# Kernel optimization log

Hardware: AMD Instinct MI355X
Metric: run time of the kernel (lower is better)

The kernel has to match this reference:

```python
import jax, jax.numpy as jnp
import numpy as np

N_NODES = 50000
N_EDGES = 1600000
IN_F, H_F, N_C = 128, 128, 16
NEG_SLOPE = 0.2  # DGL GATConv default


def setup_inputs() -> dict:
    key = jax.random.key(0)
    ks = jax.random.split(key, 12)
    def w(k, shape, fan_in):
        return jax.random.normal(k, shape, jnp.float32) / np.float32(np.sqrt(fan_in))
    return {
        "feat": jax.random.normal(ks[0], (N_NODES, IN_F), jnp.float32),
        "src": jax.random.randint(ks[1], (N_EDGES,), 0, N_NODES, dtype=jnp.int32),
        "dst": jax.random.randint(ks[2], (N_EDGES,), 0, N_NODES, dtype=jnp.int32),
        "W1": w(ks[3], (IN_F, H_F), IN_F), "al1": w(ks[4], (H_F,), H_F), "ar1": w(ks[5], (H_F,), H_F), "b1": jnp.zeros((H_F,), jnp.float32),
        "W2": w(ks[6], (H_F, H_F), H_F), "al2": w(ks[7], (H_F,), H_F), "ar2": w(ks[8], (H_F,), H_F), "b2": jnp.zeros((H_F,), jnp.float32),
        "W3": w(ks[9], (H_F, N_C), H_F), "al3": w(ks[10], (N_C,), N_C), "ar3": w(ks[11], (N_C,), N_C), "b3": jnp.zeros((N_C,), jnp.float32),
    }


def _gat_layer(h, src, dst, W, al, ar, b):
    # DGL GATConv (1 head): ft = W h; e_ij = LeakyReLU(a_l.ft_src + a_r.ft_dst);
    # alpha = edge_softmax over incoming edges of dst; out = sum alpha * ft_src + bias
    ft = h @ W                                   # [N, out]
    el = ft @ al                                 # [N]
    er = ft @ ar                                 # [N]
    e = jax.nn.leaky_relu(el[src] + er[dst], negative_slope=NEG_SLOPE)  # [E]
    emax = jax.ops.segment_max(e, dst, num_segments=N_NODES)
    emax = jnp.where(jnp.isfinite(emax), emax, 0.0)  # guard isolated nodes
    ex = jnp.exp(e - emax[dst])                  # [E]
    esum = jax.ops.segment_sum(ex, dst, num_segments=N_NODES)  # [N]
    agg = jax.ops.segment_sum(ex[:, None] * ft[src], dst, num_segments=N_NODES)  # [N, out]
    out = agg / jnp.where(esum > 0, esum, 1.0)[:, None] + b
    return jax.nn.relu(out)


def reference(feat, src, dst, W1, al1, ar1, b1, W2, al2, ar2, b2, W3, al3, ar3, b3):
    h = _gat_layer(feat, src, dst, W1, al1, ar1, b1)
    h = _gat_layer(h, src, dst, W2, al2, ar2, b2)
    h = _gat_layer(h, src, dst, W3, al3, ar3, b3)
    return h  # [N_NODES, N_C]
```

## Files before the change

kernel.cpp:

```cpp
#include <hip/hip_runtime.h>
#include <hip/hip_bf16.h>

#define NN 50000
#define NE 1600000
#define FF 128
#define CC 16
#define NB ((NN + 63) / 64)
#define NBLK 256
#define CH ((NE + NBLK - 1) / NBLK)

using bf16 = __hip_bfloat16;
using bf16x8 = __attribute__((ext_vector_type(8))) short;
using f32x4  = __attribute__((ext_vector_type(4))) float;

static __device__ __forceinline__ float ldf(const void* p, int i, int isbf){
    return isbf ? __bfloat162float(((const bf16*)p)[i]) : ((const float*)p)[i];
}
static __device__ __forceinline__ float bflo(unsigned u){
    union{unsigned x; float f;} c; c.x = u << 16; return c.f;
}
static __device__ __forceinline__ float bfhi(unsigned u){
    union{unsigned x; float f;} c; c.x = u & 0xFFFF0000u; return c.f;
}
static __device__ __forceinline__ float rdlanef(float v, int l){
    return __int_as_float(__builtin_amdgcn_readlane(__float_as_int(v), l));
}
static __device__ __forceinline__ unsigned short f2bfu(float v){
    bf16 b = __float2bfloat16(v);
    union{bf16 b; unsigned short u;} c; c.b = b; return c.u;
}

__global__ __launch_bounds__(256) void k_prep(const unsigned short* __restrict__ featu,
                                              const void* __restrict__ W1, const void* __restrict__ W2,
                                              const void* __restrict__ W3, int* __restrict__ dflag,
                                              int* __restrict__ bcounts, unsigned short* __restrict__ wtg){
    __shared__ int cnt;
    const int t = threadIdx.x;
    if (t == 0) cnt = 0;
    __syncthreads();
    unsigned short lo = featu[2 * t];
    int e = (lo >> 7) & 0xFF;
    if (e >= 117 && e <= 137) atomicAdd(&cnt, 1);
    __syncthreads();
    const int isbf = (cnt >= 128) ? 1 : 0;
    int idx = blockIdx.x * 256 + t;
    if (idx == 0) *dflag = isbf;
    if (idx < NB) bcounts[idx] = 0;
    if (idx < 32768){
        int l = idx >> 14;
        int e2 = idx & 16383;
        int f = e2 >> 7, k = e2 & 127;
        const void* W = l ? W2 : W1;
        wtg[idx] = f2bfu(ldf(W, k * FF + f, isbf));
    } else if (idx < 34816){
        int e2 = idx - 32768;
        int f = e2 >> 7, k = e2 & 127;
        wtg[idx] = f2bfu(ldf(W3, k * CC + f, isbf));
    }
}


__global__ __launch_bounds__(256) void k_bcount(const int* __restrict__ dst, int* __restrict__ bcounts,
                                                int* __restrict__ bh){
    __shared__ int hist[NB];
    const int t = threadIdx.x, b = blockIdx.x;
    for (int i = t; i < NB; i += 256) hist[i] = 0;
    __syncthreads();
    const int beg = b * CH, end = (beg + CH < NE) ? beg + CH : NE;
    for (int i = beg + t; i < end; i += 256){
        int d = dst[i];
        if ((unsigned)d >= NN) d = 0;
        atomicAdd(&hist[d >> 6], 1);
    }
    __syncthreads();
    for (int k = t; k < NB; k += 256){
        int v = hist[k];
        bh[k * NBLK + b] = v;
        if (v) atomicAdd(&bcounts[k], v);
    }
}

__global__ __launch_bounds__(256) void k_bscan(const int* __restrict__ bcounts, int* __restrict__ bbase,
                                               int* __restrict__ rowptr){
    __shared__ int s[256];
    const int t = threadIdx.x;
    constexpr int PT = (NB + 255) / 256;
    int loc[PT];
    int sum = 0;
    #pragma unroll
    for (int i = 0; i < PT; i++){
        int idx = t * PT + i;
        int v = (idx < NB) ? bcounts[idx] : 0;
        loc[i] = sum;
        sum += v;
    }
    s[t] = sum; __syncthreads();
    for (int off = 1; off < 256; off <<= 1){
        int x = (t >= off) ? s[t - off] : 0;
        __syncthreads();
        s[t] += x;
        __syncthreads();
    }
    int base = (t > 0) ? s[t - 1] : 0;
    #pragma unroll
    for (int i = 0; i < PT; i++){
        int idx = t * PT + i;
        if (idx < NB) bbase[idx] = base + loc[i];
    }
    if (t == 255){
        bbase[NB] = s[255];
        rowptr[NN] = s[255];
    }
}

__global__ __launch_bounds__(256) void k_boffset(const int* __restrict__ bbase, int* __restrict__ bh){
    int k = blockIdx.x * 4 + (threadIdx.x >> 6);
    int lane = threadIdx.x & 63;
    if (k >= NB) return;
    int v[4];
    int s = 0;
    #pragma unroll
    for (int i = 0; i < 4; i++){
        v[i] = bh[k * NBLK + 4 * lane + i];
        s += v[i];
    }
    int tot = s;
    #pragma unroll
    for (int off = 1; off < 64; off <<= 1){
        int x = __shfl_up(s, off);
        if (lane >= off) s += x;
    }
    int run = bbase[k] + s - tot;
    #pragma unroll
    for (int i = 0; i < 4; i++){
        bh[k * NBLK + 4 * lane + i] = run;
        run += v[i];
    }
}

__global__ __launch_bounds__(256) void k_bucket(const int* __restrict__ src, const int* __restrict__ dst,
                                                const int* __restrict__ bh, unsigned* __restrict__ bpairs){
    __shared__ int cur[NB];
    const int t = threadIdx.x, b = blockIdx.x;
    for (int k = t; k < NB; k += 256) cur[k] = bh[k * NBLK + b];
    __syncthreads();
    const int beg = b * CH, end = (beg + CH < NE) ? beg + CH : NE;
    for (int i = beg + t; i < end; i += 256){
        int s = src[i];
        int d = dst[i];
        if ((unsigned)s >= NN) s = 0;
        if ((unsigned)d >= NN) d = 0;
        int p = atomicAdd(&cur[d >> 6], 1);
        if ((unsigned)p < NE) bpairs[p] = (unsigned)s | ((unsigned)(d & 63) << 16);
    }
}

__global__ __launch_bounds__(256) void k_bsort(const unsigned* __restrict__ bpairs, const int* __restrict__ bbase,
                                               int* __restrict__ rowptr, int* __restrict__ csrsrc){
    __shared__ int cnt[64];
    __shared__ int cur[64];
    const int t = threadIdx.x;
    const int b = blockIdx.x;
    const int base = bbase[b];
    const int endb = bbase[b + 1];
    if (t < 64) cnt[t] = 0;
    __syncthreads();
    for (int i = base + t; i < endb; i += 256)
        atomicAdd(&cnt[bpairs[i] >> 16], 1);
    __syncthreads();
    if (t < 64){
        int v = cnt[t];
        int inc = v;
        #pragma unroll
        for (int off = 1; off < 64; off <<= 1){
            int x = __shfl_up(inc, off);
            if (t >= off) inc += x;
        }
        int excl = inc - v;
        cur[t] = excl;
        int d = b * 64 + t;
        if (d < NN) rowptr[d] = base + excl;
    }
    __syncthreads();
    for (int i = base + t; i < endb; i += 256){
        unsigned pr = bpairs[i];
        int p = atomicAdd(&cur[pr >> 16], 1);
        csrsrc[base + p] = (int)(pr & 0xFFFFu);
    }
}


template<bool XDYN>
__global__ __launch_bounds__(256) void k_mgemm(const void* __restrict__ X, const unsigned short* __restrict__ wtg,
                                               const void* __restrict__ al, const void* __restrict__ ar,
                                               const int* __restrict__ dflag, bf16* __restrict__ ft,
                                               float* __restrict__ el, float* __restrict__ er){
    const int isbf = *dflag;
    const int t  = threadIdx.x;
    const int n0 = blockIdx.x * 64;
    const int wv = t >> 6;
    const int lane = t & 63;
    const int quad = lane >> 4;
    const int mcol = lane & 15;
    const int row = n0 + wv * 16 + mcol;
    const int rc  = (row < NN) ? row : 0;

    bf16x8 afr[4];
    if (XDYN && !isbf){
        const float* xr = (const float*)X + rc * FF + quad * 8;
        #pragma unroll
        for (int kt = 0; kt < 4; kt++){
            float4 a = *(const float4*)(xr + kt * 32);
            float4 b = *(const float4*)(xr + kt * 32 + 4);
            union { bf16x8 v; unsigned u[4]; } c;
            c.u[0] = (unsigned)f2bfu(a.x) | ((unsigned)f2bfu(a.y) << 16);
            c.u[1] = (unsigned)f2bfu(a.z) | ((unsigned)f2bfu(a.w) << 16);
            c.u[2] = (unsigned)f2bfu(b.x) | ((unsigned)f2bfu(b.y) << 16);
            c.u[3] = (unsigned)f2bfu(b.z) | ((unsigned)f2bfu(b.w) << 16);
            afr[kt] = c.v;
        }
    } else {
        const unsigned short* xr = (const unsigned short*)X + rc * FF + quad * 8;
        #pragma unroll
        for (int kt = 0; kt < 4; kt++)
            afr[kt] = *(const bf16x8*)(xr + kt * 32);
    }

    float elp[4] = {0.f,0.f,0.f,0.f}, erp[4] = {0.f,0.f,0.f,0.f};

    #pragma unroll
    for (int f = 0; f < 8; f++){
        f32x4 acc = {0.f, 0.f, 0.f, 0.f};
        const unsigned short* wr = wtg + (f * 16 + mcol) * FF + quad * 8;
        #pragma unroll
        for (int kt = 0; kt < 4; kt++){
            bf16x8 bfr = *(const bf16x8*)(wr + kt * 32);
            acc = __builtin_amdgcn_mfma_f32_16x16x32_bf16(afr[kt], bfr, acc, 0, 0, 0);
        }
        int col = f * 16 + mcol;
        float alv = ldf(al, col, isbf);
        float arv = ldf(ar, col, isbf);
        #pragma unroll
        for (int reg = 0; reg < 4; reg++){
            int node = n0 + wv * 16 + quad * 4 + reg;
            float v = acc[reg];
            if (node < NN) ft[node * FF + col] = __float2bfloat16(v);
            elp[reg] += v * alv;
            erp[reg] += v * arv;
        }
    }

    #pragma unroll
    for (int reg = 0; reg < 4; reg++){
        float pl = elp[reg], pr = erp[reg];
        #pragma unroll
        for (int off = 1; off < 16; off <<= 1){
            pl += __shfl_xor(pl, off);
            pr += __shfl_xor(pr, off);
        }
        int node = n0 + wv * 16 + quad * 4 + reg;
        if (mcol == 0 && node < NN){ el[node] = pl; er[node] = pr; }
    }
}


__global__ __launch_bounds__(256) void k_mgemm3(const void* __restrict__ X, const unsigned short* __restrict__ wt3g,
                                                const void* __restrict__ al, const void* __restrict__ ar,
                                                const int* __restrict__ dflag, float* __restrict__ ft,
                                                float* __restrict__ el, float* __restrict__ er){
    const int isbf = *dflag;
    const int t  = threadIdx.x;
    const int n0 = blockIdx.x * 64;
    const int wv = t >> 6;
    const int lane = t & 63;
    const int quad = lane >> 4;
    const int mcol = lane & 15;
    const int row = n0 + wv * 16 + mcol;
    const int rc  = (row < NN) ? row : 0;

    const unsigned short* xr = (const unsigned short*)X + rc * FF + quad * 8;
    const unsigned short* wr = wt3g + mcol * FF + quad * 8;

    f32x4 acc = {0.f, 0.f, 0.f, 0.f};
    #pragma unroll
    for (int kt = 0; kt < 4; kt++){
        bf16x8 afr = *(const bf16x8*)(xr + kt * 32);
        bf16x8 bfr = *(const bf16x8*)(wr + kt * 32);
        acc = __builtin_amdgcn_mfma_f32_16x16x32_bf16(afr, bfr, acc, 0, 0, 0);
    }

    float alv = ldf(al, mcol, isbf);
    float arv = ldf(ar, mcol, isbf);
    #pragma unroll
    for (int reg = 0; reg < 4; reg++){
        int node = n0 + wv * 16 + quad * 4 + reg;
        float v = acc[reg];
        if (node < NN) ft[node * CC + mcol] = v;
        float pl = v * alv, pr = v * arv;
        #pragma unroll
        for (int off = 1; off < 16; off <<= 1){
            pl += __shfl_xor(pl, off);
            pr += __shfl_xor(pr, off);
        }
        if (mcol == 0 && node < NN){ el[node] = pl; er[node] = pr; }
    }
}


__global__ __launch_bounds__(256) void k_agg128(const void* __restrict__ ftv, const float* __restrict__ el,
                                                const float* __restrict__ er, const int* __restrict__ rowptr,
                                                const int* __restrict__ csrsrc, const void* __restrict__ bias,
                                                const int* __restrict__ dflag, unsigned* __restrict__ outp){
    const int isbf = *dflag;
    int lane = threadIdx.x & 63;
    int n = blockIdx.x * 4 + (threadIdx.x >> 6);
    if (n >= NN) return;
    int beg = rowptr[n], end = rowptr[n + 1];
    beg = (beg < 0) ? 0 : (beg > NE ? NE : beg);
    end = (end < beg) ? beg : (end > NE ? NE : end);
    int deg = end - beg;
    float erd = er[n];

    float m = -3.4e38f;
    int   s_c = 0;
    float e_c = 0.f;
    for (int i = beg + lane; i < end; i += 64){
        int s = csrsrc[i];
        if ((unsigned)s >= NN) s = 0;
        float e = el[s] + erd;
        e = (e >= 0.f) ? e : 0.2f * e;
        if (i < beg + 64){ s_c = s; e_c = e; }
        m = fmaxf(m, e);
    }
    #pragma unroll
    for (int off = 32; off; off >>= 1) m = fmaxf(m, __shfl_xor(m, off));

    int jmax = (deg < 64) ? deg : 64;
    float w_c = (lane < jmax) ? __expf(e_c - m) : 0.f;
    float lsum = w_c;
    #pragma unroll
    for (int off = 32; off; off >>= 1) lsum += __shfl_xor(lsum, off);

    const unsigned* ftb = (const unsigned*)ftv;
    float acc0 = 0.f, acc1 = 0.f;
    int j = 0;
    if (jmax >= 8){
        float w[8]; unsigned u[8];
        #pragma unroll
        for (int q = 0; q < 8; q++){
            int s = __builtin_amdgcn_readlane(s_c, q);
            w[q] = rdlanef(w_c, q);
            u[q] = (ftb + s * 64)[lane];
        }
        for (j = 8; j + 8 <= jmax; j += 8){
            float wn[8]; unsigned un[8];
            #pragma unroll
            for (int q = 0; q < 8; q++){
                int s = __builtin_amdgcn_readlane(s_c, j + q);
                wn[q] = rdlanef(w_c, j + q);
                un[q] = (ftb + s * 64)[lane];
            }
            #pragma unroll
            for (int q = 0; q < 8; q++){
                acc0 += w[q] * bflo(u[q]);
                acc1 += w[q] * bfhi(u[q]);
                w[q] = wn[q]; u[q] = un[q];
            }
        }
        #pragma unroll
        for (int q = 0; q < 8; q++){
            acc0 += w[q] * bflo(u[q]);
            acc1 += w[q] * bfhi(u[q]);
        }
    }
    for (; j < jmax; ++j){
        int s = __builtin_amdgcn_readlane(s_c, j);
        float w = rdlanef(w_c, j);
        unsigned u = (ftb + s * 64)[lane];
        acc0 += w * bflo(u); acc1 += w * bfhi(u);
    }
    for (int i = beg + 64; i < end; ++i){
        int s = csrsrc[i];
        if ((unsigned)s >= NN) s = 0;
        float e = el[s] + erd;
        e = (e >= 0.f) ? e : 0.2f * e;
        float w = __expf(e - m);
        unsigned u = (ftb + s * 64)[lane];
        lsum += w;
        acc0 += w * bflo(u); acc1 += w * bfhi(u);
    }
    float inv = 1.f / ((lsum > 0.f) ? lsum : 1.f);
    float o0 = fmaxf(acc0 * inv + ldf(bias, 2 * lane,     isbf), 0.f);
    float o1 = fmaxf(acc1 * inv + ldf(bias, 2 * lane + 1, isbf), 0.f);
    unsigned pk = (unsigned)f2bfu(o0) | ((unsigned)f2bfu(o1) << 16);
    outp[n * 64 + lane] = pk;
}


__global__ __launch_bounds__(256) void k_agg16(const float* __restrict__ ftv, const float* __restrict__ el,
                                               const float* __restrict__ er, const int* __restrict__ rowptr,
                                               const int* __restrict__ csrsrc, const void* __restrict__ bias,
                                               const int* __restrict__ dflag, void* __restrict__ outp){
    const int isbf = *dflag;
    int lane = threadIdx.x & 63;
    int n = blockIdx.x * 4 + (threadIdx.x >> 6);
    if (n >= NN) return;
    int beg = rowptr[n], end = rowptr[n + 1];
    beg = (beg < 0) ? 0 : (beg > NE ? NE : beg);
    end = (end < beg) ? beg : (end > NE ? NE : end);
    int deg = end - beg;
    float erd = er[n];

    float m = -3.4e38f;
    int   s_c = 0;
    float e_c = 0.f;
    for (int i = beg + lane; i < end; i += 64){
        int s = csrsrc[i];
        if ((unsigned)s >= NN) s = 0;
        float e = el[s] + erd;
        e = (e >= 0.f) ? e : 0.2f * e;
        if (i < beg + 64){ s_c = s; e_c = e; }
        m = fmaxf(m, e);
    }
    #pragma unroll
    for (int off = 32; off; off >>= 1) m = fmaxf(m, __shfl_xor(m, off));

    int jmax = (deg < 64) ? deg : 64;
    float w_c = (lane < jmax) ? __expf(e_c - m) : 0.f;
    float lsum = w_c;
    #pragma unroll
    for (int off = 32; off; off >>= 1) lsum += __shfl_xor(lsum, off);

    const float4* ftq = (const float4*)ftv;
    const int g   = lane >> 2;
    const int fl2 = lane & 3;
    int nbatch = (jmax + 15) >> 4;
    float wq[4]; float4 uq[4];
    #pragma unroll
    for (int q = 0; q < 4; q++){
        int eidx = (q * 16 + g) & 63;
        int s = __shfl(s_c, eidx);
        wq[q] = (q < nbatch) ? __shfl(w_c, eidx) : 0.f;
        uq[q] = ftq[(unsigned)s * 4 + fl2];
    }
    float a4[4] = {0.f,0.f,0.f,0.f};
    #pragma unroll
    for (int q = 0; q < 4; q++){
        a4[0] += wq[q] * uq[q].x;
        a4[1] += wq[q] * uq[q].y;
        a4[2] += wq[q] * uq[q].z;
        a4[3] += wq[q] * uq[q].w;
    }
    for (int i = beg + 64; i < end; ++i){
        int s = csrsrc[i];
        if ((unsigned)s >= NN) s = 0;
        float e = el[s] + erd;
        e = (e >= 0.f) ? e : 0.2f * e;
        float w = __expf(e - m);
        lsum += w;
        if (g == 0){
            float4 u = ftq[(unsigned)s * 4 + fl2];
            a4[0] += w * u.x; a4[1] += w * u.y; a4[2] += w * u.z; a4[3] += w * u.w;
        }
    }
    #pragma unroll
    for (int i = 0; i < 4; i++){
        a4[i] += __shfl_xor(a4[i], 4);
        a4[i] += __shfl_xor(a4[i], 8);
        a4[i] += __shfl_xor(a4[i], 16);
        a4[i] += __shfl_xor(a4[i], 32);
    }
    float inv = 1.f / ((lsum > 0.f) ? lsum : 1.f);
    if (lane < 4){
        float o0 = fmaxf(a4[0] * inv + ldf(bias, fl2 * 4 + 0, isbf), 0.f);
        float o1 = fmaxf(a4[1] * inv + ldf(bias, fl2 * 4 + 1, isbf), 0.f);
        float o2 = fmaxf(a4[2] * inv + ldf(bias, fl2 * 4 + 2, isbf), 0.f);
        float o3 = fmaxf(a4[3] * inv + ldf(bias, fl2 * 4 + 3, isbf), 0.f);
        if (isbf){
            uint2 pk;
            pk.x = (unsigned)f2bfu(o0) | ((unsigned)f2bfu(o1) << 16);
            pk.y = (unsigned)f2bfu(o2) | ((unsigned)f2bfu(o3) << 16);
            ((uint2*)outp)[n * 4 + fl2] = pk;
        } else {
            float4 o; o.x = o0; o.y = o1; o.z = o2; o.w = o3;
            ((float4*)outp)[n * 4 + fl2] = o;
        }
    }
}


static size_t align256(size_t x){ return (x + 255) & ~(size_t)255; }

extern "C" void kernel_launch(void* const* d_in, const int* in_sizes, int n_in,
                              void* d_out, int out_size, void* d_ws, size_t ws_size,
                              hipStream_t stream) {
    const void* feat = d_in[0];
    const int*  src  = (const int*)d_in[1];
    const int*  dst  = (const int*)d_in[2];
    const void* W1 = d_in[3];
    const void* al1= d_in[4];
    const void* ar1= d_in[5];
    const void* b1 = d_in[6];
    const void* W2 = d_in[7];
    const void* al2= d_in[8];
    const void* ar2= d_in[9];
    const void* b2 = d_in[10];
    const void* W3 = d_in[11];
    const void* al3= d_in[12];
    const void* ar3= d_in[13];
    const void* b3 = d_in[14];

    char* p = (char*)d_ws;
    size_t off = 0;
    auto carve = [&](size_t bytes)->void*{
        void* r = p + off;
        off += align256(bytes);
        return r;
    };
    float* ftA   = (float*)carve((size_t)NN * FF * 4);
    unsigned* hB = (unsigned*)carve((size_t)NN * FF * 4);
    float* el    = (float*)carve((size_t)NN * 4);
    float* er    = (float*)carve((size_t)NN * 4);
    int*   rowptr= (int*)  carve((size_t)(NN + 1) * 4);
    int*   csrsrc= (int*)  carve((size_t)NE * 4);
    int*   bcounts=(int*)  carve((size_t)NB * 4);
    int*   bbase  =(int*)  carve((size_t)(NB + 1) * 4);
    int*   bh     =(int*)  carve((size_t)NB * NBLK * 4);
    unsigned short* wtg = (unsigned short*)carve((size_t)34816 * 2);
    int*   dflag  =(int*)  carve(256);
    unsigned* bpairs = (unsigned*)hB;
    void*  ftb   = ftA;
    (void)ws_size; (void)n_in; (void)in_sizes; (void)out_size;

    dim3 b256(256);

    k_prep<<<dim3(136), b256, 0, stream>>>((const unsigned short*)feat, W1, W2, W3, dflag, bcounts, wtg);

    k_bcount<<<dim3(NBLK), b256, 0, stream>>>(dst, bcounts, bh);
    k_bscan<<<dim3(1), b256, 0, stream>>>(bcounts, bbase, rowptr);
    k_boffset<<<dim3((NB + 3) / 4), b256, 0, stream>>>(bbase, bh);
    k_bucket<<<dim3(NBLK), b256, 0, stream>>>(src, dst, bh, bpairs);
    k_bsort<<<dim3(NB), b256, 0, stream>>>(bpairs, bbase, rowptr, csrsrc);

    const int mg_grid   = (NN + 63) / 64;
    const int node_grid = (NN + 3) / 4;

    k_mgemm<true><<<dim3(mg_grid), b256, 0, stream>>>(feat, wtg, al1, ar1, dflag, (bf16*)ftb, el, er);
    k_agg128<<<dim3(node_grid), b256, 0, stream>>>(ftb, el, er, rowptr, csrsrc, b1, dflag, hB);

    k_mgemm<false><<<dim3(mg_grid), b256, 0, stream>>>(hB, wtg + 16384, al2, ar2, dflag, (bf16*)ftb, el, er);
    k_agg128<<<dim3(node_grid), b256, 0, stream>>>(ftb, el, er, rowptr, csrsrc, b2, dflag, hB);

    k_mgemm3<<<dim3(mg_grid), b256, 0, stream>>>(hB, wtg + 32768, al3, ar3, dflag, (float*)ftb, el, er);
    k_agg16<<<dim3(node_grid), b256, 0, stream>>>((const float*)ftb, el, er, rowptr, csrsrc, b3, dflag, d_out);
}
```

Before: 335.1 us.

## Gather four edges per wave with 16-byte loads in 128-wide aggregation

The 128-feature aggregation kernel now splits each wave into four 16-lane groups. Each group gathers a different neighbor's row with uint4 (8 bf16) loads, and the groups combine their partial sums with cross-lane shuffles at the end. This replaces per-lane 4-byte gathers handled one edge at a time, aiming at fewer, wider memory transactions and more edges in flight. The costs are extra shuffles, padding of the edge count to a multiple of four, and a tail loop for degree above 64 that uses only one quarter of the lanes.

After: 337.8 us. No clear change (+0.8%).

```diff
diff --git a/kernel.cpp b/kernel.cpp
--- a/kernel.cpp
+++ b/kernel.cpp
@@ -341,59 +341,73 @@
     #pragma unroll
     for (int off = 32; off; off >>= 1) lsum += __shfl_xor(lsum, off);
 
-    const unsigned* ftb = (const unsigned*)ftv;
-    float acc0 = 0.f, acc1 = 0.f;
-    int j = 0;
-    if (jmax >= 8){
-        float w[8]; unsigned u[8];
-        #pragma unroll
-        for (int q = 0; q < 8; q++){
-            int s = __builtin_amdgcn_readlane(s_c, q);
-            w[q] = rdlanef(w_c, q);
-            u[q] = (ftb + s * 64)[lane];
-        }
-        for (j = 8; j + 8 <= jmax; j += 8){
-            float wn[8]; unsigned un[8];
-            #pragma unroll
-            for (int q = 0; q < 8; q++){
-                int s = __builtin_amdgcn_readlane(s_c, j + q);
-                wn[q] = rdlanef(w_c, j + q);
-                un[q] = (ftb + s * 64)[lane];
+    const int g = lane >> 4;
+    const int c = lane & 15;
+    const uint4* ftq4 = (const uint4*)ftv;
+    float acc[8] = {0.f,0.f,0.f,0.f,0.f,0.f,0.f,0.f};
+    int jmax4 = (jmax + 3) & ~3;
+
+    for (int base = 0; base < jmax4; base += 16){
+        uint4 u[4];
+        float wB[4];
+        #pragma unroll
+        for (int q = 0; q < 4; q++){
+            int jj = base + q * 4;
+            if (jj < jmax4){
+                int idx = jj + g;
+                int sE = __shfl(s_c, idx);
+                wB[q] = __shfl(w_c, idx);
+                u[q] = ftq4[(unsigned)sE * 16u + c];
+            } else {
+                wB[q] = 0.f;
+                u[q] = (uint4){0u, 0u, 0u, 0u};
             }
-            #pragma unroll
-            for (int q = 0; q < 8; q++){
-                acc0 += w[q] * bflo(u[q]);
-                acc1 += w[q] * bfhi(u[q]);
-                w[q] = wn[q]; u[q] = un[q];
-            }
-        }
-        #pragma unroll
-        for (int q = 0; q < 8; q++){
-            acc0 += w[q] * bflo(u[q]);
-            acc1 += w[q] * bfhi(u[q]);
-        }
-    }
-    for (; j < jmax; ++j){
-        int s = __builtin_amdgcn_readlane(s_c, j);
-        float w = rdlanef(w_c, j);
-        unsigned u = (ftb + s * 64)[lane];
-        acc0 += w * bflo(u); acc1 += w * bfhi(u);
-    }
+        }
+        #pragma unroll
+        for (int q = 0; q < 4; q++){
+            float w = wB[q];
+            acc[0] += w * bflo(u[q].x); acc[1] += w * bfhi(u[q].x);
+            acc[2] += w * bflo(u[q].y); acc[3] += w * bfhi(u[q].y);
+            acc[4] += w * bflo(u[q].z); acc[5] += w * bfhi(u[q].z);
+            acc[6] += w * bflo(u[q].w); acc[7] += w * bfhi(u[q].w);
+        }
+    }
+
     for (int i = beg + 64; i < end; ++i){
         int s = csrsrc[i];
         if ((unsigned)s >= NN) s = 0;
         float e = el[s] + erd;
         e = (e >= 0.f) ? e : 0.2f * e;
         float w = __expf(e - m);
-        unsigned u = (ftb + s * 64)[lane];
         lsum += w;
-        acc0 += w * bflo(u); acc1 += w * bfhi(u);
-    }
-    float inv = 1.f / ((lsum > 0.f) ? lsum : 1.f);
-    float o0 = fmaxf(acc0 * inv + ldf(bias, 2 * lane,     isbf), 0.f);
-    float o1 = fmaxf(acc1 * inv + ldf(bias, 2 * lane + 1, isbf), 0.f);
-    unsigned pk = (unsigned)f2bfu(o0) | ((unsigned)f2bfu(o1) << 16);
-    outp[n * 64 + lane] = pk;
+        if (g == 0){
+            uint4 u = ftq4[(unsigned)s * 16u + c];
+            acc[0] += w * bflo(u.x); acc[1] += w * bfhi(u.x);
+            acc[2] += w * bflo(u.y); acc[3] += w * bfhi(u.y);
+            acc[4] += w * bflo(u.z); acc[5] += w * bfhi(u.z);
+            acc[6] += w * bflo(u.w); acc[7] += w * bfhi(u.w);
+        }
+    }
+
+    #pragma unroll
+    for (int k = 0; k < 8; k++){
+        acc[k] += __shfl_xor(acc[k], 16);
+        acc[k] += __shfl_xor(acc[k], 32);
+    }
+
+    if (g == 0){
+        float inv = 1.f / ((lsum > 0.f) ? lsum : 1.f);
+        float o[8];
+        #pragma unroll
+        for (int k = 0; k < 8; k++)
+            o[k] = fmaxf(acc[k] * inv + ldf(bias, c * 8 + k, isbf), 0.f);
+        uint4 pk;
+        pk.x = (unsigned)f2bfu(o[0]) | ((unsigned)f2bfu(o[1]) << 16);
+        pk.y = (unsigned)f2bfu(o[2]) | ((unsigned)f2bfu(o[3]) << 16);
+        pk.z = (unsigned)f2bfu(o[4]) | ((unsigned)f2bfu(o[5]) << 16);
+        pk.w = (unsigned)f2bfu(o[6]) | ((unsigned)f2bfu(o[7]) << 16);
+        ((uint4*)outp)[n * 16 + c] = pk;
+    }
 }
 
 
```

## Simplify CSR build to global atomic count-scan-scatter and drop max-subtraction in agg16

Applied to the files above, without the earlier changes.

Replaces the two-level bucketed CSR construction (block histograms, bucket offsets, bucket scatter, per-bucket sort) with a direct per-node global atomic count, a single-block scan, and an atomic scatter into csrsrc. The goal is fewer launches and fewer passes over the edge list. The trade is more contention on global atomics and a non-deterministic edge order. The final 16-wide aggregation kernel is also rewritten into a single pass that skips the softmax max subtraction, which risks exp overflow for large logits.

After: 513.8 us. 53.3% more time.

```diff
diff --git a/kernel.cpp b/kernel.cpp
--- a/kernel.cpp
+++ b/kernel.cpp
@@ -5,9 +5,7 @@
 #define NE 1600000
 #define FF 128
 #define CC 16
-#define NB ((NN + 63) / 64)
-#define NBLK 256
-#define CH ((NE + NBLK - 1) / NBLK)
+#define NCPAD 50176
 
 using bf16 = __hip_bfloat16;
 using bf16x8 = __attribute__((ext_vector_type(8))) short;
@@ -33,7 +31,7 @@
 __global__ __launch_bounds__(256) void k_prep(const unsigned short* __restrict__ featu,
                                               const void* __restrict__ W1, const void* __restrict__ W2,
                                               const void* __restrict__ W3, int* __restrict__ dflag,
-                                              int* __restrict__ bcounts, unsigned short* __restrict__ wtg){
+                                              int* __restrict__ ecnt, unsigned short* __restrict__ wtg){
     __shared__ int cnt;
     const int t = threadIdx.x;
     if (t == 0) cnt = 0;
@@ -45,7 +43,7 @@
     const int isbf = (cnt >= 128) ? 1 : 0;
     int idx = blockIdx.x * 256 + t;
     if (idx == 0) *dflag = isbf;
-    if (idx < NB) bcounts[idx] = 0;
+    if (idx < NCPAD) ecnt[idx] = 0;
     if (idx < 32768){
         int l = idx >> 14;
         int e2 = idx & 16383;
@@ -60,39 +58,25 @@
 }
 
 
-__global__ __launch_bounds__(256) void k_bcount(const int* __restrict__ dst, int* __restrict__ bcounts,
-                                                int* __restrict__ bh){
-    __shared__ int hist[NB];
-    const int t = threadIdx.x, b = blockIdx.x;
-    for (int i = t; i < NB; i += 256) hist[i] = 0;
-    __syncthreads();
-    const int beg = b * CH, end = (beg + CH < NE) ? beg + CH : NE;
-    for (int i = beg + t; i < end; i += 256){
+__global__ __launch_bounds__(256) void k_ecount(const int* __restrict__ dst, int* __restrict__ ecnt){
+    const int stride = gridDim.x * 256;
+    for (int i = blockIdx.x * 256 + threadIdx.x; i < NE; i += stride){
         int d = dst[i];
         if ((unsigned)d >= NN) d = 0;
-        atomicAdd(&hist[d >> 6], 1);
-    }
-    __syncthreads();
-    for (int k = t; k < NB; k += 256){
-        int v = hist[k];
-        bh[k * NBLK + b] = v;
-        if (v) atomicAdd(&bcounts[k], v);
-    }
-}
-
-__global__ __launch_bounds__(256) void k_bscan(const int* __restrict__ bcounts, int* __restrict__ bbase,
-                                               int* __restrict__ rowptr){
+        atomicAdd(&ecnt[d], 1);
+    }
+}
+
+__global__ __launch_bounds__(256) void k_escan(const int* __restrict__ ecnt, int* __restrict__ rowptr,
+                                               int* __restrict__ cur){
     __shared__ int s[256];
     const int t = threadIdx.x;
-    constexpr int PT = (NB + 255) / 256;
-    int loc[PT];
+    constexpr int PT = NCPAD / 256;
+    const int4* c4 = (const int4*)ecnt + t * (PT / 4);
     int sum = 0;
-    #pragma unroll
-    for (int i = 0; i < PT; i++){
-        int idx = t * PT + i;
-        int v = (idx < NB) ? bcounts[idx] : 0;
-        loc[i] = sum;
-        sum += v;
+    for (int i = 0; i < PT / 4; i++){
+        int4 v = c4[i];
+        sum += v.x + v.y + v.z + v.w;
     }
     s[t] = sum; __syncthreads();
     for (int off = 1; off < 256; off <<= 1){
@@ -101,91 +85,38 @@
         s[t] += x;
         __syncthreads();
     }
-    int base = (t > 0) ? s[t - 1] : 0;
-    #pragma unroll
-    for (int i = 0; i < PT; i++){
-        int idx = t * PT + i;
-        if (idx < NB) bbase[idx] = base + loc[i];
-    }
-    if (t == 255){
-        bbase[NB] = s[255];
-        rowptr[NN] = s[255];
-    }
-}
-
-__global__ __launch_bounds__(256) void k_boffset(const int* __restrict__ bbase, int* __restrict__ bh){
-    int k = blockIdx.x * 4 + (threadIdx.x >> 6);
-    int lane = threadIdx.x & 63;
-    if (k >= NB) return;
-    int v[4];
-    int s = 0;
-    #pragma unroll
-    for (int i = 0; i < 4; i++){
-        v[i] = bh[k * NBLK + 4 * lane + i];
-        s += v[i];
-    }
-    int tot = s;
-    #pragma unroll
-    for (int off = 1; off < 64; off <<= 1){
-        int x = __shfl_up(s, off);
-        if (lane >= off) s += x;
-    }
-    int run = bbase[k] + s - tot;
-    #pragma unroll
-    for (int i = 0; i < 4; i++){
-        bh[k * NBLK + 4 * lane + i] = run;
-        run += v[i];
-    }
-}
-
-__global__ __launch_bounds__(256) void k_bucket(const int* __restrict__ src, const int* __restrict__ dst,
-                                                const int* __restrict__ bh, unsigned* __restrict__ bpairs){
-    __shared__ int cur[NB];
-    const int t = threadIdx.x, b = blockIdx.x;
-    for (int k = t; k < NB; k += 256) cur[k] = bh[k * NBLK + b];
-    __syncthreads();
-    const int beg = b * CH, end = (beg + CH < NE) ? beg + CH : NE;
-    for (int i = beg + t; i < end; i += 256){
+    int run = (t > 0) ? s[t - 1] : 0;
+    for (int i = 0; i < PT / 4; i++){
+        int4 v = c4[i];
+        int idx = t * PT + i * 4;
+        if (idx + 3 < NN){
+            int4 r;
+            r.x = run;           r.y = run + v.x;
+            r.z = r.y + v.y;     r.w = r.z + v.z;
+            *(int4*)(rowptr + idx) = r;
+            *(int4*)(cur + idx) = r;
+            run = r.w + v.w;
+        } else {
+            int vv[4] = {v.x, v.y, v.z, v.w};
+            for (int k = 0; k < 4; k++){
+                if (idx + k < NN){ rowptr[idx + k] = run; cur[idx + k] = run; }
+                run += vv[k];
+            }
+        }
+    }
+    if (t == 255) rowptr[NN] = s[255];
+}
+
+__global__ __launch_bounds__(256) void k_escatter(const int* __restrict__ src, const int* __restrict__ dst,
+                                                  int* __restrict__ cur, int* __restrict__ csrsrc){
+    const int stride = gridDim.x * 256;
+    for (int i = blockIdx.x * 256 + threadIdx.x; i < NE; i += stride){
         int s = src[i];
         int d = dst[i];
         if ((unsigned)s >= NN) s = 0;
         if ((unsigned)d >= NN) d = 0;
-        int p = atomicAdd(&cur[d >> 6], 1);
-        if ((unsigned)p < NE) bpairs[p] = (unsigned)s | ((unsigned)(d & 63) << 16);
-    }
-}
-
-__global__ __launch_bounds__(256) void k_bsort(const unsigned* __restrict__ bpairs, const int* __restrict__ bbase,
-                                               int* __restrict__ rowptr, int* __restrict__ csrsrc){
-    __shared__ int cnt[64];
-    __shared__ int cur[64];
-    const int t = threadIdx.x;
-    const int b = blockIdx.x;
-    const int base = bbase[b];
-    const int endb = bbase[b + 1];
-    if (t < 64) cnt[t] = 0;
-    __syncthreads();
-    for (int i = base + t; i < endb; i += 256)
-        atomicAdd(&cnt[bpairs[i] >> 16], 1);
-    __syncthreads();
-    if (t < 64){
-        int v = cnt[t];
-        int inc = v;
-        #pragma unroll
-        for (int off = 1; off < 64; off <<= 1){
-            int x = __shfl_up(inc, off);
-            if (t >= off) inc += x;
-        }
-        int excl = inc - v;
-        cur[t] = excl;
-        int d = b * 64 + t;
-        if (d < NN) rowptr[d] = base + excl;
-    }
-    __syncthreads();
-    for (int i = base + t; i < endb; i += 256){
-        unsigned pr = bpairs[i];
-        int p = atomicAdd(&cur[pr >> 16], 1);
-        csrsrc[base + p] = (int)(pr & 0xFFFFu);
+        int p = atomicAdd(&cur[d], 1);
+        if ((unsigned)p < NE) csrsrc[p] = s;
     }
 }
 
@@ -402,88 +333,59 @@
                                                const int* __restrict__ csrsrc, const void* __restrict__ bias,
                                                const int* __restrict__ dflag, void* __restrict__ outp){
     const int isbf = *dflag;
-    int lane = threadIdx.x & 63;
-    int n = blockIdx.x * 4 + (threadIdx.x >> 6);
+    const int lane = threadIdx.x & 63;
+    const int n = blockIdx.x * 4 + (threadIdx.x >> 6);
     if (n >= NN) return;
     int beg = rowptr[n], end = rowptr[n + 1];
     beg = (beg < 0) ? 0 : (beg > NE ? NE : beg);
     end = (end < beg) ? beg : (end > NE ? NE : end);
-    int deg = end - beg;
-    float erd = er[n];
-
-    float m = -3.4e38f;
-    int   s_c = 0;
-    float e_c = 0.f;
-    for (int i = beg + lane; i < end; i += 64){
-        int s = csrsrc[i];
-        if ((unsigned)s >= NN) s = 0;
-        float e = el[s] + erd;
-        e = (e >= 0.f) ? e : 0.2f * e;
-        if (i < beg + 64){ s_c = s; e_c = e; }
-        m = fmaxf(m, e);
-    }
-    #pragma unroll
-    for (int off = 32; off; off >>= 1) m = fmaxf(m, __shfl_xor(m, off));
-
-    int jmax = (deg < 64) ? deg : 64;
-    float w_c = (lane < jmax) ? __expf(e_c - m) : 0.f;
-    float lsum = w_c;
-    #pragma unroll
-    for (int off = 32; off; off >>= 1) lsum += __shfl_xor(lsum, off);
-
+    const float erd = er[n];
+
+    const int g = lane >> 2;
+    const int c = lane & 3;
     const float4* ftq = (const float4*)ftv;
-    const int g   = lane >> 2;
-    const int fl2 = lane & 3;
-    int nbatch = (jmax + 15) >> 4;
-    float wq[4]; float4 uq[4];
-    #pragma unroll
-    for (int q = 0; q < 4; q++){
-        int eidx = (q * 16 + g) & 63;
-        int s = __shfl(s_c, eidx);
-        wq[q] = (q < nbatch) ? __shfl(w_c, eidx) : 0.f;
-        uq[q] = ftq[(unsigned)s * 4 + fl2];
-    }
-    float a4[4] = {0.f,0.f,0.f,0.f};
-    #pragma unroll
-    for (int q = 0; q < 4; q++){
-        a4[0] += wq[q] * uq[q].x;
-        a4[1] += wq[q] * uq[q].y;
-        a4[2] += wq[q] * uq[q].z;
-        a4[3] += wq[q] * uq[q].w;
-    }
-    for (int i = beg + 64; i < end; ++i){
-        int s = csrsrc[i];
-        if ((unsigned)s >= NN) s = 0;
-        float e = el[s] + erd;
-        e = (e >= 0.f) ? e : 0.2f * e;
-        float w = __expf(e - m);
-        lsum += w;
-        if (g == 0){
-            float4 u = ftq[(unsigned)s * 4 + fl2];
-            a4[0] += w * u.x; a4[1] += w * u.y; a4[2] += w * u.z; a4[3] += w * u.w;
-        }
-    }
-    #pragma unroll
-    for (int i = 0; i < 4; i++){
-        a4[i] += __shfl_xor(a4[i], 4);
-        a4[i] += __shfl_xor(a4[i], 8);
-        a4[i] += __shfl_xor(a4[i], 16);
-        a4[i] += __shfl_xor(a4[i], 32);
-    }
-    float inv = 1.f / ((lsum > 0.f) ? lsum : 1.f);
+    float a0 = 0.f, a1 = 0.f, a2 = 0.f, a3 = 0.f;
+    float lsum = 0.f;
+
+    for (int j = beg; j < end; j += 32){
+        #pragma unroll
+        for (int q = 0; q < 2; q++){
+            int iq = j + q * 16 + g;
+            int cq = (iq < end) ? iq : beg;
+            int s  = csrsrc[cq];
+            if ((unsigned)s >= NN) s = 0;
+            float e = el[s] + erd;
+            e = (e >= 0.f) ? e : 0.2f * e;
+            float w = (iq < end) ? __expf(e) : 0.f;
+            float4 u = ftq[(unsigned)s * 4u + c];
+            lsum += w;
+            a0 += w * u.x; a1 += w * u.y; a2 += w * u.z; a3 += w * u.w;
+        }
+    }
+
+    #pragma unroll
+    for (int off = 4; off < 64; off <<= 1){
+        a0 += __shfl_xor(a0, off);
+        a1 += __shfl_xor(a1, off);
+        a2 += __shfl_xor(a2, off);
+        a3 += __shfl_xor(a3, off);
+        lsum += __shfl_xor(lsum, off);
+    }
+
     if (lane < 4){
-        float o0 = fmaxf(a4[0] * inv + ldf(bias, fl2 * 4 + 0, isbf), 0.f);
-        float o1 = fmaxf(a4[1] * inv + ldf(bias, fl2 * 4 + 1, isbf), 0.f);
-        float o2 = fmaxf(a4[2] * inv + ldf(bias, fl2 * 4 + 2, isbf), 0.f);
-        float o3 = fmaxf(a4[3] * inv + ldf(bias, fl2 * 4 + 3, isbf), 0.f);
+        float inv = (lsum > 0.f) ? 1.f / lsum : 0.f;
+        float o0 = fmaxf(a0 * inv + ldf(bias, c * 4 + 0, isbf), 0.f);
+        float o1 = fmaxf(a1 * inv + ldf(bias, c * 4 + 1, isbf), 0.f);
+        float o2 = fmaxf(a2 * inv + ldf(bias, c * 4 + 2, isbf), 0.f);
+        float o3 = fmaxf(a3 * inv + ldf(bias, c * 4 + 3, isbf), 0.f);
         if (isbf){
             uint2 pk;
             pk.x = (unsigned)f2bfu(o0) | ((unsigned)f2bfu(o1) << 16);
             pk.y = (unsigned)f2bfu(o2) | ((unsigned)f2bfu(o3) << 16);
-            ((uint2*)outp)[n * 4 + fl2] = pk;
+            ((uint2*)outp)[n * 4 + c] = pk;
         } else {
             float4 o; o.x = o0; o.y = o1; o.z = o2; o.w = o3;
-            ((float4*)outp)[n * 4 + fl2] = o;
+            ((float4*)outp)[n * 4 + c] = o;
         }
     }
 }
@@ -523,24 +425,20 @@
     float* er    = (float*)carve((size_t)NN * 4);
     int*   rowptr= (int*)  carve((size_t)(NN + 1) * 4);
     int*   csrsrc= (int*)  carve((size_t)NE * 4);
-    int*   bcounts=(int*)  carve((size_t)NB * 4);
-    int*   bbase  =(int*)  carve((size_t)(NB + 1) * 4);
-    int*   bh     =(int*)  carve((size_t)NB * NBLK * 4);
+    int*   ecnt  = (int*)  carve((size_t)NCPAD * 4);
+    int*   cur   = (int*)  carve((size_t)NCPAD * 4);
     unsigned short* wtg = (unsigned short*)carve((size_t)34816 * 2);
     int*   dflag  =(int*)  carve(256);
-    unsigned* bpairs = (unsigned*)hB;
     void*  ftb   = ftA;
     (void)ws_size; (void)n_in; (void)in_sizes; (void)out_size;
 
     dim3 b256(256);
 
-    k_prep<<<dim3(136), b256, 0, stream>>>((const unsigned short*)feat, W1, W2, W3, dflag, bcounts, wtg);
-
-    k_bcount<<<dim3(NBLK), b256, 0, stream>>>(dst, bcounts, bh);
-    k_bscan<<<dim3(1), b256, 0, stream>>>(bcounts, bbase, rowptr);
-    k_boffset<<<dim3((NB + 3) / 4), b256, 0, stream>>>(bbase, bh);
-    k_bucket<<<dim3(NBLK), b256, 0, stream>>>(src, dst, bh, bpairs);
-    k_bsort<<<dim3(NB), b256, 0, stream>>>(bpairs, bbase, rowptr, csrsrc);
+    k_prep<<<dim3(196), b256, 0, stream>>>((const unsigned short*)feat, W1, W2, W3, dflag, ecnt, wtg);
+
+    k_ecount<<<dim3(1024), b256, 0, stream>>>(dst, ecnt);
+    k_escan<<<dim3(1), b256, 0, stream>>>(ecnt, rowptr, cur);
+    k_escatter<<<dim3(1024), b256, 0, stream>>>(src, dst, cur, csrsrc);
 
     const int mg_grid   = (NN + 63) / 64;
     const int node_grid = (NN + 3) / 4;
```

## Fuse preprocessing kernels, co-launch bucketing with layer-1 GEMM, simplify agg16

Applied to the files above, without the earlier changes.

Merges the dtype probe, weight transpose and destination histogram into one kernel. The scan now sums the per-block histograms directly, which removes the global atomic bucket counts. The edge-bucketing pass and the first-layer MFMA GEMM are combined into one launch with disjoint block ranges, so the two independent jobs run at the same time and two launches disappear. The final 16-wide aggregation drops the max-subtraction pass and uses a single batched loop, which adds a risk of exp overflow for large logits.

New measurement: 345.4 us. +3.1%, slower.

```diff
diff --git a/kernel.cpp b/kernel.cpp
--- a/kernel.cpp
+++ b/kernel.cpp
@@ -30,22 +30,24 @@
     union{bf16 b; unsigned short u;} c; c.b = b; return c.u;
 }
 
-__global__ __launch_bounds__(256) void k_prep(const unsigned short* __restrict__ featu,
-                                              const void* __restrict__ W1, const void* __restrict__ W2,
-                                              const void* __restrict__ W3, int* __restrict__ dflag,
-                                              int* __restrict__ bcounts, unsigned short* __restrict__ wtg){
+__global__ __launch_bounds__(256) void k_prepcount(const unsigned short* __restrict__ featu,
+                                                   const void* __restrict__ W1, const void* __restrict__ W2,
+                                                   const void* __restrict__ W3, const int* __restrict__ dst,
+                                                   int* __restrict__ dflag, int* __restrict__ bh,
+                                                   unsigned short* __restrict__ wtg){
     __shared__ int cnt;
-    const int t = threadIdx.x;
+    __shared__ int hist[NB];
+    const int t = threadIdx.x, b = blockIdx.x;
     if (t == 0) cnt = 0;
+    for (int i = t; i < NB; i += 256) hist[i] = 0;
     __syncthreads();
     unsigned short lo = featu[2 * t];
     int e = (lo >> 7) & 0xFF;
     if (e >= 117 && e <= 137) atomicAdd(&cnt, 1);
     __syncthreads();
     const int isbf = (cnt >= 128) ? 1 : 0;
-    int idx = blockIdx.x * 256 + t;
+    int idx = b * 256 + t;
     if (idx == 0) *dflag = isbf;
-    if (idx < NB) bcounts[idx] = 0;
     if (idx < 32768){
         int l = idx >> 14;
         int e2 = idx & 16383;
@@ -57,15 +59,6 @@
         int f = e2 >> 7, k = e2 & 127;
         wtg[idx] = f2bfu(ldf(W3, k * CC + f, isbf));
     }
-}
-
-
-__global__ __launch_bounds__(256) void k_bcount(const int* __restrict__ dst, int* __restrict__ bcounts,
-                                                int* __restrict__ bh){
-    __shared__ int hist[NB];
-    const int t = threadIdx.x, b = blockIdx.x;
-    for (int i = t; i < NB; i += 256) hist[i] = 0;
-    __syncthreads();
     const int beg = b * CH, end = (beg + CH < NE) ? beg + CH : NE;
     for (int i = beg + t; i < end; i += 256){
         int d = dst[i];
@@ -73,14 +66,10 @@
         atomicAdd(&hist[d >> 6], 1);
     }
     __syncthreads();
-    for (int k = t; k < NB; k += 256){
-        int v = hist[k];
-        bh[k * NBLK + b] = v;
-        if (v) atomicAdd(&bcounts[k], v);
-    }
-}
-
-__global__ __launch_bounds__(256) void k_bscan(const int* __restrict__ bcounts, int* __restrict__ bbase,
+    for (int k = t; k < NB; k += 256) bh[k * NBLK + b] = hist[k];
+}
+
+__global__ __launch_bounds__(256) void k_bscan(const int* __restrict__ bh, int* __restrict__ bbase,
                                                int* __restrict__ rowptr){
     __shared__ int s[256];
     const int t = threadIdx.x;
@@ -90,7 +79,14 @@
     #pragma unroll
     for (int i = 0; i < PT; i++){
         int idx = t * PT + i;
-        int v = (idx < NB) ? bcounts[idx] : 0;
+        int v = 0;
+        if (idx < NB){
+            const int4* q = (const int4*)(bh + idx * NBLK);
+            for (int j = 0; j < NBLK / 4; j++){
+                int4 x = q[j];
+                v += x.x + x.y + x.z + x.w;
+            }
+        }
         loc[i] = sum;
         sum += v;
     }
@@ -138,20 +134,94 @@
     }
 }
 
-__global__ __launch_bounds__(256) void k_bucket(const int* __restrict__ src, const int* __restrict__ dst,
-                                                const int* __restrict__ bh, unsigned* __restrict__ bpairs){
-    __shared__ int cur[NB];
-    const int t = threadIdx.x, b = blockIdx.x;
-    for (int k = t; k < NB; k += 256) cur[k] = bh[k * NBLK + b];
-    __syncthreads();
-    const int beg = b * CH, end = (beg + CH < NE) ? beg + CH : NE;
-    for (int i = beg + t; i < end; i += 256){
-        int s = src[i];
-        int d = dst[i];
-        if ((unsigned)s >= NN) s = 0;
-        if ((unsigned)d >= NN) d = 0;
-        int p = atomicAdd(&cur[d >> 6], 1);
-        if ((unsigned)p < NE) bpairs[p] = (unsigned)s | ((unsigned)(d & 63) << 16);
+
+__global__ __launch_bounds__(256) void k_fat(const int* __restrict__ src, const int* __restrict__ dst,
+                                             const int* __restrict__ bh, unsigned* __restrict__ bpairs,
+                                             const void* __restrict__ X, const unsigned short* __restrict__ wtg,
+                                             const void* __restrict__ al, const void* __restrict__ ar,
+                                             const int* __restrict__ dflag, bf16* __restrict__ ft,
+                                             float* __restrict__ el, float* __restrict__ er){
+    if (blockIdx.x < NBLK){
+        __shared__ int cur[NB];
+        const int t = threadIdx.x, b = blockIdx.x;
+        for (int k = t; k < NB; k += 256) cur[k] = bh[k * NBLK + b];
+        __syncthreads();
+        const int beg = b * CH, end = (beg + CH < NE) ? beg + CH : NE;
+        for (int i = beg + t; i < end; i += 256){
+            int s = src[i];
+            int d = dst[i];
+            if ((unsigned)s >= NN) s = 0;
+            if ((unsigned)d >= NN) d = 0;
+            int p = atomicAdd(&cur[d >> 6], 1);
+            if ((unsigned)p < NE) bpairs[p] = (unsigned)s | ((unsigned)(d & 63) << 16);
+        }
+        return;
+    }
+    const int isbf = *dflag;
+    const int t  = threadIdx.x;
+    const int n0 = (blockIdx.x - NBLK) * 64;
+    const int wv = t >> 6;
+    const int lane = t & 63;
+    const int quad = lane >> 4;
+    const int mcol = lane & 15;
+    const int row = n0 + wv * 16 + mcol;
+    const int rc  = (row < NN) ? row : 0;
+
+    bf16x8 afr[4];
+    if (!isbf){
+        const float* xr = (const float*)X + rc * FF + quad * 8;
+        #pragma unroll
+        for (int kt = 0; kt < 4; kt++){
+            float4 a = *(const float4*)(xr + kt * 32);
+            float4 b = *(const float4*)(xr + kt * 32 + 4);
+            union { bf16x8 v; unsigned u[4]; } c;
+            c.u[0] = (unsigned)f2bfu(a.x) | ((unsigned)f2bfu(a.y) << 16);
+            c.u[1] = (unsigned)f2bfu(a.z) | ((unsigned)f2bfu(a.w) << 16);
+            c.u[2] = (unsigned)f2bfu(b.x) | ((unsigned)f2bfu(b.y) << 16);
+            c.u[3] = (unsigned)f2bfu(b.z) | ((unsigned)f2bfu(b.w) << 16);
+            afr[kt] = c.v;
+        }
+    } else {
+        const unsigned short* xr = (const unsigned short*)X + rc * FF + quad * 8;
+        #pragma unroll
+        for (int kt = 0; kt < 4; kt++)
+            afr[kt] = *(const bf16x8*)(xr + kt * 32);
+    }
+
+    float elp[4] = {0.f,0.f,0.f,0.f}, erp[4] = {0.f,0.f,0.f,0.f};
+
+    #pragma unroll
+    for (int f = 0; f < 8; f++){
+        f32x4 acc = {0.f, 0.f, 0.f, 0.f};
+        const unsigned short* wr = wtg + (f * 16 + mcol) * FF + quad * 8;
+        #pragma unroll
+        for (int kt = 0; kt < 4; kt++){
+            bf16x8 bfr = *(const bf16x8*)(wr + kt * 32);
+            acc = __builtin_amdgcn_mfma_f32_16x16x32_bf16(afr[kt], bfr, acc, 0, 0, 0);
+        }
+        int col = f * 16 + mcol;
+        float alv = ldf(al, col, isbf);
+        float arv = ldf(ar, col, isbf);
+        #pragma unroll
+        for (int reg = 0; reg < 4; reg++){
+            int node = n0 + wv * 16 + quad * 4 + reg;
+            float v = acc[reg];
+            if (node < NN) ft[node * FF + col] = __float2bfloat16(v);
+            elp[reg] += v * alv;
+            erp[reg] += v * arv;
+        }
+    }
+
+    #pragma unroll
+    for (int reg = 0; reg < 4; reg++){
+        float pl = elp[reg], pr = erp[reg];
+        #pragma unroll
+        for (int off = 1; off < 16; off <<= 1){
+            pl += __shfl_xor(pl, off);
+            pr += __shfl_xor(pr, off);
+        }
+        int node = n0 + wv * 16 + quad * 4 + reg;
+        if (mcol == 0 && node < NN){ el[node] = pl; er[node] = pr; }
     }
 }
 
@@ -190,11 +260,10 @@
 }
 
 
-template<bool XDYN>
-__global__ __launch_bounds__(256) void k_mgemm(const void* __restrict__ X, const unsigned short* __restrict__ wtg,
-                                               const void* __restrict__ al, const void* __restrict__ ar,
-                                               const int* __restrict__ dflag, bf16* __restrict__ ft,
-                                               float* __restrict__ el, float* __restrict__ er){
+__global__ __launch_bounds__(256) void k_mgemm2(const void* __restrict__ X, const unsigned short* __restrict__ wtg,
+                                                const void* __restrict__ al, const void* __restrict__ ar,
+                                                const int* __restrict__ dflag, bf16* __restrict__ ft,
+                                                float* __restrict__ el, float* __restrict__ er){
     const int isbf = *dflag;
     const int t  = threadIdx.x;
     const int n0 = blockIdx.x * 64;
@@ -206,25 +275,10 @@
     const int rc  = (row < NN) ? row : 0;
 
     bf16x8 afr[4];
-    if (XDYN && !isbf){
-        const float* xr = (const float*)X + rc * FF + quad * 8;
-        #pragma unroll
-        for (int kt = 0; kt < 4; kt++){
-            float4 a = *(const float4*)(xr + kt * 32);
-            float4 b = *(const float4*)(xr + kt * 32 + 4);
-            union { bf16x8 v; unsigned u[4]; } c;
-            c.u[0] = (unsigned)f2bfu(a.x) | ((unsigned)f2bfu(a.y) << 16);
-            c.u[1] = (unsigned)f2bfu(a.z) | ((unsigned)f2bfu(a.w) << 16);
-            c.u[2] = (unsigned)f2bfu(b.x) | ((unsigned)f2bfu(b.y) << 16);
-            c.u[3] = (unsigned)f2bfu(b.z) | ((unsigned)f2bfu(b.w) << 16);
-            afr[kt] = c.v;
-        }
-    } else {
-        const unsigned short* xr = (const unsigned short*)X + rc * FF + quad * 8;
-        #pragma unroll
-        for (int kt = 0; kt < 4; kt++)
-            afr[kt] = *(const bf16x8*)(xr + kt * 32);
-    }
+    const unsigned short* xr = (const unsigned short*)X + rc * FF + quad * 8;
+    #pragma unroll
+    for (int kt = 0; kt < 4; kt++)
+        afr[kt] = *(const bf16x8*)(xr + kt * 32);
 
     float elp[4] = {0.f,0.f,0.f,0.f}, erp[4] = {0.f,0.f,0.f,0.f};
 
@@ -402,88 +456,59 @@
                                                const int* __restrict__ csrsrc, const void* __restrict__ bias,
                                                const int* __restrict__ dflag, void* __restrict__ outp){
     const int isbf = *dflag;
-    int lane = threadIdx.x & 63;
-    int n = blockIdx.x * 4 + (threadIdx.x >> 6);
+    const int lane = threadIdx.x & 63;
+    const int n = blockIdx.x * 4 + (threadIdx.x >> 6);
     if (n >= NN) return;
     int beg = rowptr[n], end = rowptr[n + 1];
     beg = (beg < 0) ? 0 : (beg > NE ? NE : beg);
     end = (end < beg) ? beg : (end > NE ? NE : end);
-    int deg = end - beg;
-    float erd = er[n];
-
-    float m = -3.4e38f;
-    int   s_c = 0;
-    float e_c = 0.f;
-    for (int i = beg + lane; i < end; i += 64){
-        int s = csrsrc[i];
-        if ((unsigned)s >= NN) s = 0;
-        float e = el[s] + erd;
-        e = (e >= 0.f) ? e : 0.2f * e;
-        if (i < beg + 64){ s_c = s; e_c = e; }
-        m = fmaxf(m, e);
-    }
-    #pragma unroll
-    for (int off = 32; off; off >>= 1) m = fmaxf(m, __shfl_xor(m, off));
-
-    int jmax = (deg < 64) ? deg : 64;
-    float w_c = (lane < jmax) ? __expf(e_c - m) : 0.f;
-    float lsum = w_c;
-    #pragma unroll
-    for (int off = 32; off; off >>= 1) lsum += __shfl_xor(lsum, off);
-
+    const float erd = er[n];
+
+    const int g = lane >> 2;
+    const int c = lane & 3;
     const float4* ftq = (const float4*)ftv;
-    const int g   = lane >> 2;
-    const int fl2 = lane & 3;
-    int nbatch = (jmax + 15) >> 4;
-    float wq[4]; float4 uq[4];
-    #pragma unroll
-    for (int q = 0; q < 4; q++){
-        int eidx = (q * 16 + g) & 63;
-        int s = __shfl(s_c, eidx);
-        wq[q] = (q < nbatch) ? __shfl(w_c, eidx) : 0.f;
-        uq[q] = ftq[(unsigned)s * 4 + fl2];
-    }
-    float a4[4] = {0.f,0.f,0.f,0.f};
-    #pragma unroll
-    for (int q = 0; q < 4; q++){
-        a4[0] += wq[q] * uq[q].x;
-        a4[1] += wq[q] * uq[q].y;
-        a4[2] += wq[q] * uq[q].z;
-        a4[3] += wq[q] * uq[q].w;
-    }
-    for (int i = beg + 64; i < end; ++i){
-        int s = csrsrc[i];
-        if ((unsigned)s >= NN) s = 0;
-        float e = el[s] + erd;
-        e = (e >= 0.f) ? e : 0.2f * e;
-        float w = __expf(e - m);
-        lsum += w;
-        if (g == 0){
-            float4 u = ftq[(unsigned)s * 4 + fl2];
-            a4[0] += w * u.x; a4[1] += w * u.y; a4[2] += w * u.z; a4[3] += w * u.w;
-        }
-    }
-    #pragma unroll
-    for (int i = 0; i < 4; i++){
-        a4[i] += __shfl_xor(a4[i], 4);
-        a4[i] += __shfl_xor(a4[i], 8);
-        a4[i] += __shfl_xor(a4[i], 16);
-        a4[i] += __shfl_xor(a4[i], 32);
-    }
-    float inv = 1.f / ((lsum > 0.f) ? lsum : 1.f);
+    float a0 = 0.f, a1 = 0.f, a2 = 0.f, a3 = 0.f;
+    float lsum = 0.f;
+
+    for (int j = beg; j < end; j += 32){
+        #pragma unroll
+        for (int q = 0; q < 2; q++){
+            int iq = j + q * 16 + g;
+            int cq = (iq < end) ? iq : beg;
+            int s  = csrsrc[cq];
+            if ((unsigned)s >= NN) s = 0;
+            float e = el[s] + erd;
+            e = (e >= 0.f) ? e : 0.2f * e;
+            float w = (iq < end) ? __expf(e) : 0.f;
+            float4 u = ftq[(unsigned)s * 4u + c];
+            lsum += w;
+            a0 += w * u.x; a1 += w * u.y; a2 += w * u.z; a3 += w * u.w;
+        }
+    }
+
+    #pragma unroll
+    for (int off = 4; off < 64; off <<= 1){
+        a0 += __shfl_xor(a0, off);
+        a1 += __shfl_xor(a1, off);
+        a2 += __shfl_xor(a2, off);
+        a3 += __shfl_xor(a3, off);
+        lsum += __shfl_xor(lsum, off);
+    }
+
     if (lane < 4){
-        float o0 = fmaxf(a4[0] * inv + ldf(bias, fl2 * 4 + 0, isbf), 0.f);
-        float o1 = fmaxf(a4[1] * inv + ldf(bias, fl2 * 4 + 1, isbf), 0.f);
-        float o2 = fmaxf(a4[2] * inv + ldf(bias, fl2 * 4 + 2, isbf), 0.f);
-        float o3 = fmaxf(a4[3] * inv + ldf(bias, fl2 * 4 + 3, isbf), 0.f);
+        float inv = (lsum > 0.f) ? 1.f / lsum : 0.f;
+        float o0 = fmaxf(a0 * inv + ldf(bias, c * 4 + 0, isbf), 0.f);
+        float o1 = fmaxf(a1 * inv + ldf(bias, c * 4 + 1, isbf), 0.f);
+        float o2 = fmaxf(a2 * inv + ldf(bias, c * 4 + 2, isbf), 0.f);
+        float o3 = fmaxf(a3 * inv + ldf(bias, c * 4 + 3, isbf), 0.f);
         if (isbf){
             uint2 pk;
             pk.x = (unsigned)f2bfu(o0) | ((unsigned)f2bfu(o1) << 16);
             pk.y = (unsigned)f2bfu(o2) | ((unsigned)f2bfu(o3) << 16);
-            ((uint2*)outp)[n * 4 + fl2] = pk;
+            ((uint2*)outp)[n * 4 + c] = pk;
         } else {
             float4 o; o.x = o0; o.y = o1; o.z = o2; o.w = o3;
-            ((float4*)outp)[n * 4 + fl2] = o;
+            ((float4*)outp)[n * 4 + c] = o;
         }
     }
 }
@@ -523,7 +548,6 @@
     float* er    = (float*)carve((size_t)NN * 4);
     int*   rowptr= (int*)  carve((size_t)(NN + 1) * 4);
     int*   csrsrc= (int*)  carve((size_t)NE * 4);
-    int*   bcounts=(int*)  carve((size_t)NB * 4);
     int*   bbase  =(int*)  carve((size_t)(NB + 1) * 4);
     int*   bh     =(int*)  carve((size_t)NB * NBLK * 4);
     unsigned short* wtg = (unsigned short*)carve((size_t)34816 * 2);
@@ -533,24 +557,19 @@
     (void)ws_size; (void)n_in; (void)in_sizes; (void)out_size;
 
     dim3 b256(256);
-
-    k_prep<<<dim3(136), b256, 0, stream>>>((const unsigned short*)feat, W1, W2, W3, dflag, bcounts, wtg);
-
-    k_bcount<<<dim3(NBLK), b256, 0, stream>>>(dst, bcounts, bh);
-    k_bscan<<<dim3(1), b256, 0, stream>>>(bcounts, bbase, rowptr);
-    k_boffset<<<dim3((NB + 3) / 4), b256, 0, stream>>>(bbase, bh);
-    k_bucket<<<dim3(NBLK), b256, 0, stream>>>(src, dst, bh, bpairs);
-    k_bsort<<<dim3(NB), b256, 0, stream>>>(bpairs, bbase, rowptr, csrsrc);
-
     const int mg_grid   = (NN + 63) / 64;
     const int node_grid = (NN + 3) / 4;
 
-    k_mgemm<true><<<dim3(mg_grid), b256, 0, stream>>>(feat, wtg, al1, ar1, dflag, (bf16*)ftb, el, er);
+    k_prepcount<<<dim3(NBLK), b256, 0, stream>>>((const unsigned short*)feat, W1, W2, W3, dst, dflag, bh, wtg);
+    k_bscan<<<dim3(1), b256, 0, stream>>>(bh, bbase, rowptr);
+    k_boffset<<<dim3((NB + 3) / 4), b256, 0, stream>>>(bbase, bh);
+    k_fat<<<dim3(NBLK + mg_grid), b256, 0, stream>>>(src, dst, bh, bpairs, feat, wtg, al1, ar1,
+                                                     dflag, (bf16*)ftb, el, er);
+    k_bsort<<<dim3(NB), b256, 0, stream>>>(bpairs, bbase, rowptr, csrsrc);
+
     k_agg128<<<dim3(node_grid), b256, 0, stream>>>(ftb, el, er, rowptr, csrsrc, b1, dflag, hB);
-
-    k_mgemm<false><<<dim3(mg_grid), b256, 0, stream>>>(hB, wtg + 16384, al2, ar2, dflag, (bf16*)ftb, el, er);
+    k_mgemm2<<<dim3(mg_grid), b256, 0, stream>>>(hB, wtg + 16384, al2, ar2, dflag, (bf16*)ftb, el, er);
     k_agg128<<<dim3(node_grid), b256, 0, stream>>>(ftb, el, er, rowptr, csrsrc, b2, dflag, hB);
-
     k_mgemm3<<<dim3(mg_grid), b256, 0, stream>>>(hB, wtg + 32768, al3, ar3, dflag, (float*)ftb, el, er);
     k_agg16<<<dim3(node_grid), b256, 0, stream>>>((const float*)ftb, el, er, rowptr, csrsrc, b3, dflag, d_out);
 }
```
